# Performance work log

Hardware: AMD Instinct MI355X
Metric: run time of the kernel (lower is better)

The kernel has to match this reference:

```python
import jax, jax.numpy as jnp
import numpy as np

N_NODES = 100000
N_EDGES = 1600000


def setup_inputs() -> dict:
    key = jax.random.key(0)
    k1, k2, k3, k4 = jax.random.split(key, 4)
    x = jax.random.normal(k1, (N_NODES, 128), dtype=jnp.float32)
    edge_index = jax.random.randint(k2, (2, N_EDGES), 0, N_NODES, dtype=jnp.int64)
    # Glorot-ish init for weights
    W1 = jax.random.normal(k3, (128, 128), dtype=jnp.float32) * (1.0 / np.sqrt(128))
    b1 = jnp.zeros((128,), dtype=jnp.float32)
    W2 = jax.random.normal(k4, (128, 64), dtype=jnp.float32) * (1.0 / np.sqrt(128))
    b2 = jnp.zeros((64,), dtype=jnp.float32)
    return {"x": x, "edge_index": edge_index, "W1": W1, "b1": b1, "W2": W2, "b2": b2}


def _gcn_conv(x, src, dst, W, b):
    """PyG GCNConv: h = W x; symmetric deg^-1/2 norm over edges (incl. self-loops); scatter-add; + bias."""
    n = x.shape[0]
    h = x @ W  # [N, out]
    ones = jnp.ones(src.shape[0], dtype=h.dtype)
    deg = jax.ops.segment_sum(ones, dst, num_segments=n)  # in-degree incl self-loops
    dinv = jax.lax.rsqrt(jnp.maximum(deg, 1e-12))
    norm = dinv[src] * dinv[dst]  # [E+N]
    msg = h[src] * norm[:, None]  # [E+N, out] gather
    out = jax.ops.segment_sum(msg, dst, num_segments=n)  # scatter-add
    return out + b


def reference(x, edge_index, W1, b1, W2, b2):
    n = x.shape[0]
    loop = jnp.arange(n, dtype=edge_index.dtype)
    src = jnp.concatenate([edge_index[0], loop])  # add self-loops
    dst = jnp.concatenate([edge_index[1], loop])
    h = jax.nn.relu(_gcn_conv(x, src, dst, W1, b1))
    # dropout is identity in eval mode
    return _gcn_conv(h, src, dst, W2, b2)
```

## Files before the change

kernel.cpp:

```cpp
#include <hip/hip_runtime.h>
#include <hip/hip_bf16.h>

#define THREADS 256
#define BSHIFT 9
#define BIN_CHUNK 4096
#define KP 136

typedef __attribute__((ext_vector_type(8))) short bf16x8;
typedef __attribute__((ext_vector_type(8))) unsigned short u16x8;
typedef __attribute__((ext_vector_type(4))) float f32x4;


__device__ inline unsigned short f2bf(float f) {
    unsigned int u = __float_as_uint(f);
    unsigned int r = (u + 0x7fffu + ((u >> 16) & 1u)) >> 16;
    return (unsigned short)r;
}

__device__ inline float2 bf2_to_f2(unsigned int u) {
    float2 r;
    r.x = __uint_as_float(u << 16);
    r.y = __uint_as_float(u & 0xffff0000u);
    return r;
}

__device__ inline void accum_row(float* acc, uint4 v) {
    float2 a = bf2_to_f2(v.x), b = bf2_to_f2(v.y), c = bf2_to_f2(v.z), d = bf2_to_f2(v.w);
    acc[0] += a.x; acc[1] += a.y; acc[2] += b.x; acc[3] += b.y;
    acc[4] += c.x; acc[5] += c.y; acc[6] += d.x; acc[7] += d.y;
}

__device__ inline void accum_row_scaled(float* acc, uint4 v, float s) {
    float2 a = bf2_to_f2(v.x), b = bf2_to_f2(v.y), c = bf2_to_f2(v.z), d = bf2_to_f2(v.w);
    acc[0] = fmaf(s, a.x, acc[0]); acc[1] = fmaf(s, a.y, acc[1]);
    acc[2] = fmaf(s, b.x, acc[2]); acc[3] = fmaf(s, b.y, acc[3]);
    acc[4] = fmaf(s, c.x, acc[4]); acc[5] = fmaf(s, c.y, acc[5]);
    acc[6] = fmaf(s, d.x, acc[6]); acc[7] = fmaf(s, d.y, acc[7]);
}

__device__ inline bf16x8 load_bfrag(const float* __restrict__ W, int ldn, int k0, int col) {
    bf16x8 b;
#pragma unroll
    for (int i = 0; i < 8; ++i) b[i] = (short)f2bf(W[(size_t)(k0 + i) * ldn + col]);
    return b;
}


__global__ __launch_bounds__(256) void k_bin_gemm1(const int* __restrict__ src,
                                                   const int* __restrict__ dst,
                                                   int* __restrict__ bcur,
                                                   unsigned int* __restrict__ binned,
                                                   int E, int NB, int cap,
                                                   const float* __restrict__ x,
                                                   const float* __restrict__ W1,
                                                   unsigned short* __restrict__ h,
                                                   int M, int nbin) {
    __shared__ __align__(16) short As[64 * KP];
    const int t = threadIdx.x;

    if ((int)blockIdx.x < nbin) {
        int* bcnt = (int*)As;
        int* bres = bcnt + 256;
        bcnt[t] = 0;
        __syncthreads();
        int base = blockIdx.x * BIN_CHUNK;
        int sv[16], dv[16];
#pragma unroll
        for (int i = 0; i < 16; ++i) {
            int e = base + t + i * 256;
            if (e < E) {
                sv[i] = src[e];
                dv[i] = dst[e];
                atomicAdd(&bcnt[dv[i] >> BSHIFT], 1);
            } else {
                dv[i] = -1;
            }
        }
        __syncthreads();
        if (t < NB) {
            int old = bcnt[t] ? atomicAdd(&bcur[t], bcnt[t]) : 0;
            bres[t] = t * cap + old;
        }
        __syncthreads();
#pragma unroll
        for (int i = 0; i < 16; ++i) {
            if (dv[i] >= 0) {
                int b = dv[i] >> BSHIFT;
                int pos = atomicAdd(&bres[b], 1);
                if (pos < (b + 1) * cap)
                    binned[pos] = ((unsigned int)(dv[i] & 511) << 23) | (unsigned int)sv[i];
            }
        }
        return;
    }

    const int m0 = ((int)blockIdx.x - nbin) * 64;
    {
        int ar = t >> 5;
        int ac = (t & 31) * 4;
#pragma unroll
        for (int rb = 0; rb < 64; rb += 8) {
            int lrow = rb + ar;
            int row = m0 + lrow;
            ushort4 sv = make_ushort4(0, 0, 0, 0);
            if (row < M) {
                float4 v = *(const float4*)(x + (size_t)row * 128 + ac);
                sv.x = f2bf(v.x); sv.y = f2bf(v.y); sv.z = f2bf(v.z); sv.w = f2bf(v.w);
            }
            *(ushort4*)&As[lrow * KP + ac] = sv;
        }
    }
    __syncthreads();

    const int w = t >> 6;
    const int lane = t & 63;
    const int lm = lane & 15;
    const int qd = lane >> 4;
    const int n0w = w * 32;

    f32x4 acc[4][2];
#pragma unroll
    for (int mi = 0; mi < 4; ++mi)
#pragma unroll
        for (int ni = 0; ni < 2; ++ni) acc[mi][ni] = (f32x4){0.f, 0.f, 0.f, 0.f};

#pragma unroll
    for (int ks = 0; ks < 4; ++ks) {
        bf16x8 b0 = load_bfrag(W1, 128, ks * 32 + qd * 8, n0w + lm);
        bf16x8 b1 = load_bfrag(W1, 128, ks * 32 + qd * 8, n0w + 16 + lm);
#pragma unroll
        for (int mi = 0; mi < 4; ++mi) {
            bf16x8 a = *(const bf16x8*)&As[(mi * 16 + lm) * KP + ks * 32 + qd * 8];
            acc[mi][0] = __builtin_amdgcn_mfma_f32_16x16x32_bf16(a, b0, acc[mi][0], 0, 0, 0);
            acc[mi][1] = __builtin_amdgcn_mfma_f32_16x16x32_bf16(a, b1, acc[mi][1], 0, 0, 0);
        }
    }

#pragma unroll
    for (int mi = 0; mi < 4; ++mi) {
#pragma unroll
        for (int ni = 0; ni < 2; ++ni) {
            int col = n0w + ni * 16 + lm;
#pragma unroll
            for (int r = 0; r < 4; ++r) {
                int lrow = mi * 16 + qd * 4 + r;
                int row = m0 + lrow;
                if (row < M) h[(size_t)row * 128 + col] = f2bf(acc[mi][ni][r]);
            }
        }
    }
}

__global__ __launch_bounds__(256) void k_node_place(const unsigned int* __restrict__ binned,
                                                    const int* __restrict__ bcur, int cap,
                                                    int* __restrict__ rp,
                                                    int* __restrict__ deg,
                                                    float* __restrict__ dinv,
                                                    int* __restrict__ eperm, int N) {
    __shared__ int lc[512];
    __shared__ int s[256];
    int b = blockIdx.x;
    int t = threadIdx.x;
    int beg = b * cap;
    int end = beg + min(bcur[b], cap);
    int d0 = b << BSHIFT;
    lc[t] = 0;
    lc[t + 256] = 0;
    __syncthreads();
    for (int j = beg + t; j < end; j += 256) atomicAdd(&lc[binned[j] >> 23], 1);
    __syncthreads();
    int a = lc[2 * t], c = lc[2 * t + 1];
    int pair = a + c;
    s[t] = pair;
    __syncthreads();
    for (int off = 1; off < 256; off <<= 1) {
        int add = (t >= off) ? s[t - off] : 0;
        __syncthreads();
        s[t] += add;
        __syncthreads();
    }
    int excl = s[t] - pair;
    int st0 = beg + excl, st1 = st0 + a;
    int node0 = d0 + 2 * t;
    if (node0 < N) {
        rp[node0] = st0;
        deg[node0] = a;
        dinv[node0] = rsqrtf((float)a + 1.0f);
    }
    if (node0 + 1 < N) {
        rp[node0 + 1] = st1;
        deg[node0 + 1] = c;
        dinv[node0 + 1] = rsqrtf((float)c + 1.0f);
    }
    __syncthreads();
    lc[2 * t] = st0;
    lc[2 * t + 1] = st1;
    __syncthreads();
    for (int j = beg + t; j < end; j += 256) {
        unsigned int p = binned[j];
        int pos = atomicAdd(&lc[p >> 23], 1);
        eperm[pos] = (int)(p & 0x7fffffu);
    }
}


__global__ __launch_bounds__(256, 8) void k_gather_gemm2(const int* __restrict__ rp,
                                                         const int* __restrict__ deg,
                                                         const int* __restrict__ eperm,
                                                         const float* __restrict__ dinv,
                                                         const uint4* __restrict__ h4,
                                                         const float* __restrict__ b1,
                                                         const float* __restrict__ W2,
                                                         unsigned short* __restrict__ h2,
                                                         int n) {
    __shared__ __align__(16) short As[64 * KP];

    const int t = threadIdx.x;
    const int lane = t & 63;
    const int l16 = lane & 15;
    const int gbase = lane & 48;
    const int m0 = blockIdx.x * 64;

#pragma unroll 1
    for (int r = 0; r < 4; ++r) {
        const int lrow = r * 16 + ((t >> 6) << 2) + (lane >> 4);
        const int node = m0 + lrow;
        const bool valid = node < n;

        int beg = 0, end = 0;
        float dv_self = 0.f;
        if (valid) {
            beg = rp[node];
            end = beg + deg[node];
            dv_self = dinv[node];
        }

        float acc[8];
#pragma unroll
        for (int i = 0; i < 8; ++i) acc[i] = 0.f;
        if (valid) accum_row_scaled(acc, h4[(size_t)node * 16 + l16], dv_self);

        for (int j = beg; j < end; j += 16) {
            int cnt = end - j;
            if (cnt > 16) cnt = 16;
            int ep = eperm[j + (l16 < cnt ? l16 : cnt - 1)];
            float dvv = dinv[ep];
            int k = 0;
            for (; k + 4 <= cnt; k += 4) {
                int i0 = __shfl(ep, gbase + k);
                int i1 = __shfl(ep, gbase + k + 1);
                int i2 = __shfl(ep, gbase + k + 2);
                int i3 = __shfl(ep, gbase + k + 3);
                float d0 = __shfl(dvv, gbase + k);
                float d1 = __shfl(dvv, gbase + k + 1);
                float d2 = __shfl(dvv, gbase + k + 2);
                float d3 = __shfl(dvv, gbase + k + 3);
                uint4 v0 = h4[(size_t)i0 * 16 + l16];
                uint4 v1 = h4[(size_t)i1 * 16 + l16];
                uint4 v2 = h4[(size_t)i2 * 16 + l16];
                uint4 v3 = h4[(size_t)i3 * 16 + l16];
                accum_row_scaled(acc, v0, d0);
                accum_row_scaled(acc, v1, d1);
                accum_row_scaled(acc, v2, d2);
                accum_row_scaled(acc, v3, d3);
            }
            for (; k < cnt; ++k) {
                int i0 = __shfl(ep, gbase + k);
                float d0 = __shfl(dvv, gbase + k);
                uint4 v0 = h4[(size_t)i0 * 16 + l16];
                accum_row_scaled(acc, v0, d0);
            }
        }

        float4 bb0 = ((const float4*)b1)[l16 * 2];
        float4 bb1 = ((const float4*)b1)[l16 * 2 + 1];
        u16x8 s;
        s[0] = f2bf(fmaxf(fmaf(dv_self, acc[0], bb0.x), 0.f));
        s[1] = f2bf(fmaxf(fmaf(dv_self, acc[1], bb0.y), 0.f));
        s[2] = f2bf(fmaxf(fmaf(dv_self, acc[2], bb0.z), 0.f));
        s[3] = f2bf(fmaxf(fmaf(dv_self, acc[3], bb0.w), 0.f));
        s[4] = f2bf(fmaxf(fmaf(dv_self, acc[4], bb1.x), 0.f));
        s[5] = f2bf(fmaxf(fmaf(dv_self, acc[5], bb1.y), 0.f));
        s[6] = f2bf(fmaxf(fmaf(dv_self, acc[6], bb1.z), 0.f));
        s[7] = f2bf(fmaxf(fmaf(dv_self, acc[7], bb1.w), 0.f));
        *(u16x8*)&As[lrow * KP + l16 * 8] = s;
    }
    __syncthreads();
    __builtin_amdgcn_sched_barrier(0);

    const int w = t >> 6;
    const int lm = lane & 15;
    const int qd = lane >> 4;
    const int n0w = w * 16;
    const int col = n0w + lm;

    f32x4 c4[4];
#pragma unroll
    for (int mi = 0; mi < 4; ++mi) c4[mi] = (f32x4){0.f, 0.f, 0.f, 0.f};

#pragma unroll
    for (int ks = 0; ks < 4; ++ks) {
        bf16x8 b = load_bfrag(W2, 64, ks * 32 + qd * 8, col);
#pragma unroll
        for (int mi = 0; mi < 4; ++mi) {
            bf16x8 a = *(const bf16x8*)&As[(mi * 16 + lm) * KP + ks * 32 + qd * 8];
            c4[mi] = __builtin_amdgcn_mfma_f32_16x16x32_bf16(a, b, c4[mi], 0, 0, 0);
        }
    }

#pragma unroll
    for (int mi = 0; mi < 4; ++mi) {
#pragma unroll
        for (int r = 0; r < 4; ++r) {
            int lrow = mi * 16 + qd * 4 + r;
            int row = m0 + lrow;
            if (row < n) h2[(size_t)row * 64 + col] = f2bf(dinv[row] * c4[mi][r]);
        }
    }
}

__global__ __launch_bounds__(256) void k_gather64(const int* __restrict__ rp,
                                                  const int* __restrict__ deg,
                                                  const int* __restrict__ eperm,
                                                  const float* __restrict__ dinv,
                                                  const uint4* __restrict__ h4,
                                                  const float* __restrict__ bias,
                                                  float* __restrict__ out, int n) {
    const int t = threadIdx.x;
    const int lane = t & 63;
    const int l8 = lane & 7;
    const int gbase = lane & 56;
    const int node = blockIdx.x * 32 + (t >> 6) * 8 + (lane >> 3);
    const bool valid = node < n;

    int beg = 0, end = 0;
    if (valid) {
        beg = rp[node];
        end = beg + deg[node];
    }

    float acc[8];
#pragma unroll
    for (int i = 0; i < 8; ++i) acc[i] = 0.f;
    if (valid) accum_row(acc, h4[(size_t)node * 8 + l8]);

    int j = beg;
    for (; j + 16 <= end; j += 16) {
        int ep0 = eperm[j + l8];
        int ep1 = eperm[j + 8 + l8];
        int idx[16];
#pragma unroll
        for (int k = 0; k < 8; ++k) idx[k] = __shfl(ep0, gbase + k);
#pragma unroll
        for (int k = 0; k < 8; ++k) idx[8 + k] = __shfl(ep1, gbase + k);
        uint4 v[16];
#pragma unroll
        for (int k = 0; k < 16; ++k) v[k] = h4[(size_t)idx[k] * 8 + l8];
#pragma unroll
        for (int k = 0; k < 16; ++k) accum_row(acc, v[k]);
    }
    int cnt = end - j;
    if (cnt >= 8) {
        int ep = eperm[j + l8];
        int idx[8];
#pragma unroll
        for (int k = 0; k < 8; ++k) idx[k] = __shfl(ep, gbase + k);
        uint4 v[8];
#pragma unroll
        for (int k = 0; k < 8; ++k) v[k] = h4[(size_t)idx[k] * 8 + l8];
#pragma unroll
        for (int k = 0; k < 8; ++k) accum_row(acc, v[k]);
        j += 8;
        cnt -= 8;
    }
    if (cnt > 0) {
        int ep = eperm[j + (l8 < cnt ? l8 : cnt - 1)];
        int k = 0;
        for (; k + 4 <= cnt; k += 4) {
            int i0 = __shfl(ep, gbase + k);
            int i1 = __shfl(ep, gbase + k + 1);
            int i2 = __shfl(ep, gbase + k + 2);
            int i3 = __shfl(ep, gbase + k + 3);
            uint4 v0 = h4[(size_t)i0 * 8 + l8];
            uint4 v1 = h4[(size_t)i1 * 8 + l8];
            uint4 v2 = h4[(size_t)i2 * 8 + l8];
            uint4 v3 = h4[(size_t)i3 * 8 + l8];
            accum_row(acc, v0);
            accum_row(acc, v1);
            accum_row(acc, v2);
            accum_row(acc, v3);
        }
        for (; k < cnt; ++k) {
            int i0 = __shfl(ep, gbase + k);
            uint4 v0 = h4[(size_t)i0 * 8 + l8];
            accum_row(acc, v0);
        }
    }

    if (valid) {
        float dv = dinv[node];
        float4 b0 = ((const float4*)bias)[l8 * 2];
        float4 b1 = ((const float4*)bias)[l8 * 2 + 1];
        float4 o0, o1;
        o0.x = dv * acc[0] + b0.x; o0.y = dv * acc[1] + b0.y;
        o0.z = dv * acc[2] + b0.z; o0.w = dv * acc[3] + b0.w;
        o1.x = dv * acc[4] + b1.x; o1.y = dv * acc[5] + b1.y;
        o1.z = dv * acc[6] + b1.z; o1.w = dv * acc[7] + b1.w;
        float4* orow = (float4*)(out + (size_t)node * 64);
        orow[l8 * 2] = o0;
        orow[l8 * 2 + 1] = o1;
    }
}


extern "C" void kernel_launch(void* const* d_in, const int* in_sizes, int n_in,
                              void* d_out, int out_size, void* d_ws, size_t ws_size,
                              hipStream_t stream) {
    const float* x  = (const float*)d_in[0];
    const int*   ei = (const int*)d_in[1];
    const float* W1 = (const float*)d_in[2];
    const float* b1 = (const float*)d_in[3];
    const float* W2 = (const float*)d_in[4];
    const float* b2 = (const float*)d_in[5];
    float* out = (float*)d_out;

    const int N = in_sizes[0] / 128;
    const int E = in_sizes[1] / 2;
    const int* src = ei;
    const int* dst = ei + E;
    const int NB = (N + 511) >> BSHIFT;
    const int cap = (E + NB - 1) / NB + ((E / NB) >> 2) + 1024;

    char* ws = (char*)d_ws;
    size_t off = 0;
    auto carve = [&](size_t bytes) -> void* {
        void* p = ws + off;
        off = (off + bytes + 255) & ~(size_t)255;
        return p;
    };
    float* dinv = (float*)carve((size_t)N * 4);
    int*   rp   = (int*)carve((size_t)N * 4);
    int*   deg  = (int*)carve((size_t)N * 4);
    int*   bcur = (int*)carve(256 * 4);
    unsigned int* binned = (unsigned int*)carve((size_t)NB * cap * 4);
    int*   eperm = (int*)carve((size_t)NB * cap * 4);
    unsigned short* h  = (unsigned short*)carve((size_t)N * 128 * 2);
    unsigned short* h2 = (unsigned short*)carve((size_t)N * 128 * 2);

    const int gMm = (N + 63) / 64;
    const int nbin = (E + BIN_CHUNK - 1) / BIN_CHUNK;

    hipMemsetAsync(bcur, 0, 256 * sizeof(int), stream);
    k_bin_gemm1<<<nbin + gMm, THREADS, 0, stream>>>(src, dst, bcur, binned, E, NB, cap,
                                                    x, W1, h, N, nbin);
    k_node_place<<<NB, THREADS, 0, stream>>>(binned, bcur, cap, rp, deg, dinv, eperm, N);

    k_gather_gemm2<<<gMm, THREADS, 0, stream>>>(rp, deg, eperm, dinv, (const uint4*)h, b1, W2, h2, N);

    k_gather64<<<(N + 31) / 32, THREADS, 0, stream>>>(rp, deg, eperm, dinv, (const uint4*)h2, b2, out, N);
}
```

Before: 266.7 us.

## Shrink gather-GEMM2 tile to 16 rows and pre-transpose W2 to bf16

The fused gather+GEMM2 kernel now handles 16 nodes per block instead of 64 (one gather pass instead of four sequential ones), with a smaller LDS tile and one MFMA chain per wave. W2 is transposed and converted to bf16 once, by an extra block in the node-place kernel, so B fragments become a single vector load. This targets tail latency and low parallelism in the gather phase, at the cost of reloading W2 fragments in four times as many blocks. The h2 workspace is also trimmed to its real size.

```diff
diff --git a/kernel.cpp b/kernel.cpp
--- a/kernel.cpp
+++ b/kernel.cpp
@@ -156,11 +156,21 @@
                                                     int* __restrict__ rp,
                                                     int* __restrict__ deg,
                                                     float* __restrict__ dinv,
-                                                    int* __restrict__ eperm, int N) {
+                                                    int* __restrict__ eperm, int N,
+                                                    const float* __restrict__ W2,
+                                                    unsigned short* __restrict__ W2t, int NB) {
+    int b = blockIdx.x;
+    int t = threadIdx.x;
+    if (b == NB) {
+        for (int i = t; i < 64 * 128; i += 256) {
+            int nn = i >> 7;
+            int kk = i & 127;
+            W2t[i] = f2bf(W2[(size_t)kk * 64 + nn]);
+        }
+        return;
+    }
     __shared__ int lc[512];
     __shared__ int s[256];
-    int b = blockIdx.x;
-    int t = threadIdx.x;
     int beg = b * cap;
     int end = beg + min(bcur[b], cap);
     int d0 = b << BSHIFT;
@@ -204,74 +214,72 @@
 }
 
 
-__global__ __launch_bounds__(256, 8) void k_gather_gemm2(const int* __restrict__ rp,
-                                                         const int* __restrict__ deg,
-                                                         const int* __restrict__ eperm,
-                                                         const float* __restrict__ dinv,
-                                                         const uint4* __restrict__ h4,
-                                                         const float* __restrict__ b1,
-                                                         const float* __restrict__ W2,
-                                                         unsigned short* __restrict__ h2,
-                                                         int n) {
-    __shared__ __align__(16) short As[64 * KP];
+__global__ __launch_bounds__(256) void k_gather_gemm2(const int* __restrict__ rp,
+                                                      const int* __restrict__ deg,
+                                                      const int* __restrict__ eperm,
+                                                      const float* __restrict__ dinv,
+                                                      const uint4* __restrict__ h4,
+                                                      const float* __restrict__ b1,
+                                                      const unsigned short* __restrict__ W2t,
+                                                      unsigned short* __restrict__ h2,
+                                                      int n) {
+    __shared__ __align__(16) short As[16 * KP];
 
     const int t = threadIdx.x;
     const int lane = t & 63;
     const int l16 = lane & 15;
     const int gbase = lane & 48;
-    const int m0 = blockIdx.x * 64;
-
-#pragma unroll 1
-    for (int r = 0; r < 4; ++r) {
-        const int lrow = r * 16 + ((t >> 6) << 2) + (lane >> 4);
-        const int node = m0 + lrow;
-        const bool valid = node < n;
-
-        int beg = 0, end = 0;
-        float dv_self = 0.f;
-        if (valid) {
-            beg = rp[node];
-            end = beg + deg[node];
-            dv_self = dinv[node];
-        }
-
-        float acc[8];
-#pragma unroll
-        for (int i = 0; i < 8; ++i) acc[i] = 0.f;
-        if (valid) accum_row_scaled(acc, h4[(size_t)node * 16 + l16], dv_self);
-
-        for (int j = beg; j < end; j += 16) {
-            int cnt = end - j;
-            if (cnt > 16) cnt = 16;
-            int ep = eperm[j + (l16 < cnt ? l16 : cnt - 1)];
-            float dvv = dinv[ep];
-            int k = 0;
-            for (; k + 4 <= cnt; k += 4) {
-                int i0 = __shfl(ep, gbase + k);
-                int i1 = __shfl(ep, gbase + k + 1);
-                int i2 = __shfl(ep, gbase + k + 2);
-                int i3 = __shfl(ep, gbase + k + 3);
-                float d0 = __shfl(dvv, gbase + k);
-                float d1 = __shfl(dvv, gbase + k + 1);
-                float d2 = __shfl(dvv, gbase + k + 2);
-                float d3 = __shfl(dvv, gbase + k + 3);
-                uint4 v0 = h4[(size_t)i0 * 16 + l16];
-                uint4 v1 = h4[(size_t)i1 * 16 + l16];
-                uint4 v2 = h4[(size_t)i2 * 16 + l16];
-                uint4 v3 = h4[(size_t)i3 * 16 + l16];
-                accum_row_scaled(acc, v0, d0);
-                accum_row_scaled(acc, v1, d1);
-                accum_row_scaled(acc, v2, d2);
-                accum_row_scaled(acc, v3, d3);
-            }
-            for (; k < cnt; ++k) {
-                int i0 = __shfl(ep, gbase + k);
-                float d0 = __shfl(dvv, gbase + k);
-                uint4 v0 = h4[(size_t)i0 * 16 + l16];
-                accum_row_scaled(acc, v0, d0);
-            }
-        }
-
+    const int m0 = blockIdx.x * 16;
+    const int lrow = (t >> 6) * 4 + (lane >> 4);
+    const int node = m0 + lrow;
+    const bool valid = node < n;
+
+    int beg = 0, end = 0;
+    float dv_self = 0.f;
+    if (valid) {
+        beg = rp[node];
+        end = beg + deg[node];
+        dv_self = dinv[node];
+    }
+
+    float acc[8];
+#pragma unroll
+    for (int i = 0; i < 8; ++i) acc[i] = 0.f;
+    if (valid) accum_row_scaled(acc, h4[(size_t)node * 16 + l16], dv_self);
+
+    for (int j = beg; j < end; j += 16) {
+        int cnt = end - j;
+        if (cnt > 16) cnt = 16;
+        int ep = eperm[j + (l16 < cnt ? l16 : cnt - 1)];
+        float dvv = dinv[ep];
+        int k = 0;
+        for (; k + 4 <= cnt; k += 4) {
+            int i0 = __shfl(ep, gbase + k);
+            int i1 = __shfl(ep, gbase + k + 1);
+            int i2 = __shfl(ep, gbase + k + 2);
+            int i3 = __shfl(ep, gbase + k + 3);
+            float d0 = __shfl(dvv, gbase + k);
+            float d1 = __shfl(dvv, gbase + k + 1);
+            float d2 = __shfl(dvv, gbase + k + 2);
+            float d3 = __shfl(dvv, gbase + k + 3);
+            uint4 v0 = h4[(size_t)i0 * 16 + l16];
+            uint4 v1 = h4[(size_t)i1 * 16 + l16];
+            uint4 v2 = h4[(size_t)i2 * 16 + l16];
+            uint4 v3 = h4[(size_t)i3 * 16 + l16];
+            accum_row_scaled(acc, v0, d0);
+            accum_row_scaled(acc, v1, d1);
+            accum_row_scaled(acc, v2, d2);
+            accum_row_scaled(acc, v3, d3);
+        }
+        for (; k < cnt; ++k) {
+            int i0 = __shfl(ep, gbase + k);
+            float d0 = __shfl(dvv, gbase + k);
+            uint4 v0 = h4[(size_t)i0 * 16 + l16];
+            accum_row_scaled(acc, v0, d0);
+        }
+    }
+
+    {
         float4 bb0 = ((const float4*)b1)[l16 * 2];
         float4 bb1 = ((const float4*)b1)[l16 * 2 + 1];
         u16x8 s;
@@ -286,36 +294,24 @@
         *(u16x8*)&As[lrow * KP + l16 * 8] = s;
     }
     __syncthreads();
-    __builtin_amdgcn_sched_barrier(0);
 
     const int w = t >> 6;
     const int lm = lane & 15;
     const int qd = lane >> 4;
-    const int n0w = w * 16;
-    const int col = n0w + lm;
-
-    f32x4 c4[4];
-#pragma unroll
-    for (int mi = 0; mi < 4; ++mi) c4[mi] = (f32x4){0.f, 0.f, 0.f, 0.f};
-
+    const int col = w * 16 + lm;
+
+    f32x4 c4 = (f32x4){0.f, 0.f, 0.f, 0.f};
 #pragma unroll
     for (int ks = 0; ks < 4; ++ks) {
-        bf16x8 b = load_bfrag(W2, 64, ks * 32 + qd * 8, col);
-#pragma unroll
-        for (int mi = 0; mi < 4; ++mi) {
-            bf16x8 a = *(const bf16x8*)&As[(mi * 16 + lm) * KP + ks * 32 + qd * 8];
-            c4[mi] = __builtin_amdgcn_mfma_f32_16x16x32_bf16(a, b, c4[mi], 0, 0, 0);
-        }
-    }
-
-#pragma unroll
-    for (int mi = 0; mi < 4; ++mi) {
-#pragma unroll
-        for (int r = 0; r < 4; ++r) {
-            int lrow = mi * 16 + qd * 4 + r;
-            int row = m0 + lrow;
-            if (row < n) h2[(size_t)row * 64 + col] = f2bf(dinv[row] * c4[mi][r]);
-        }
+        bf16x8 b = *(const bf16x8*)&W2t[(size_t)col * 128 + ks * 32 + qd * 8];
+        bf16x8 a = *(const bf16x8*)&As[lm * KP + ks * 32 + qd * 8];
+        c4 = __builtin_amdgcn_mfma_f32_16x16x32_bf16(a, b, c4, 0, 0, 0);
+    }
+
+#pragma unroll
+    for (int r = 0; r < 4; ++r) {
+        int row = m0 + qd * 4 + r;
+        if (row < n) h2[(size_t)row * 64 + col] = f2bf(dinv[row] * c4[r]);
     }
 }
 
@@ -444,8 +440,9 @@
     int*   bcur = (int*)carve(256 * 4);
     unsigned int* binned = (unsigned int*)carve((size_t)NB * cap * 4);
     int*   eperm = (int*)carve((size_t)NB * cap * 4);
-    unsigned short* h  = (unsigned short*)carve((size_t)N * 128 * 2);
-    unsigned short* h2 = (unsigned short*)carve((size_t)N * 128 * 2);
+    unsigned short* h   = (unsigned short*)carve((size_t)N * 128 * 2);
+    unsigned short* h2  = (unsigned short*)carve((size_t)N * 64 * 2);
+    unsigned short* W2t = (unsigned short*)carve(64 * 128 * 2);
 
     const int gMm = (N + 63) / 64;
     const int nbin = (E + BIN_CHUNK - 1) / BIN_CHUNK;
@@ -453,9 +450,11 @@
     hipMemsetAsync(bcur, 0, 256 * sizeof(int), stream);
     k_bin_gemm1<<<nbin + gMm, THREADS, 0, stream>>>(src, dst, bcur, binned, E, NB, cap,
                                                     x, W1, h, N, nbin);
-    k_node_place<<<NB, THREADS, 0, stream>>>(binned, bcur, cap, rp, deg, dinv, eperm, N);
-
-    k_gather_gemm2<<<gMm, THREADS, 0, stream>>>(rp, deg, eperm, dinv, (const uint4*)h, b1, W2, h2, N);
+    k_node_place<<<NB + 1, THREADS, 0, stream>>>(binned, bcur, cap, rp, deg, dinv, eperm, N,
+                                                 W2, W2t, NB);
+
+    k_gather_gemm2<<<(N + 15) / 16, THREADS, 0, stream>>>(rp, deg, eperm, dinv, (const uint4*)h,
+                                                          b1, W2t, h2, N);
 
     k_gather64<<<(N + 31) / 32, THREADS, 0, stream>>>(rp, deg, eperm, dinv, (const uint4*)h2, b2, out, N);
 }
```

Result: faster. 258.0 us (-3.3%).
